# Performance work log

Hardware: AMD Instinct MI355X
Metric: run time of the kernel (lower is better)

Reference implementation:

```python
import jax, jax.numpy as jnp
import numpy as np

N_USERS = 120000
N_ITEMS = 80000
N_NODES = N_USERS + N_ITEMS
D = 64
H = 2
DK = 32
DV = 32
N_LAYERS = 3
N_EDGES = 1280000
B = 4096
TEMPERATURE = 1.0


def setup_inputs() -> dict:
    key = jax.random.key(0)
    ks = jax.random.split(key, 11)
    glorot = lambda k, shape: jax.random.normal(k, shape, dtype=jnp.float32) * np.sqrt(2.0 / (shape[0] + int(np.prod(shape[1:]))))
    return {
        "edge_src": jax.random.randint(ks[0], (N_EDGES,), 0, N_NODES, dtype=jnp.int32),
        "edge_dst": jax.random.randint(ks[1], (N_EDGES,), 0, N_NODES, dtype=jnp.int32),
        # normalized adjacency values (positive, small) like D^-1/2 A D^-1/2 entries
        "edge_val": jax.random.uniform(ks[2], (N_EDGES,), dtype=jnp.float32) * 0.2,
        "U_emb": jax.random.normal(ks[3], (N_USERS, D), dtype=jnp.float32) * 0.01,
        "V_emb": jax.random.normal(ks[4], (N_ITEMS, D), dtype=jnp.float32) * 0.01,
        "Wq": glorot(ks[5], (D, H, DK)),
        "Wk": glorot(ks[6], (D, H, DK)),
        "Wv": glorot(ks[7], (D, H, DV)),
        "Wo": glorot(ks[8], (H * DV, D)),
        "u": jax.random.randint(ks[9], (B,), 0, N_USERS, dtype=jnp.int32),
        "i": jax.random.randint(ks[10], (B,), 0, N_ITEMS, dtype=jnp.int32),
    }


def reference(edge_src, edge_dst, edge_val, U_emb, V_emb, Wq, Wk, Wv, Wo, u, i):
    E0 = jnp.concatenate([U_emb, V_emb], axis=0)  # (N, d)

    # LightGCN propagation: E_{l+1} = A_norm @ E_l via edge-list scatter-add
    def prop(E, _):
        msg = edge_val[:, None] * E[edge_src]                      # (E, d) gather
        En = jax.ops.segment_sum(msg, edge_dst, num_segments=N_NODES)  # (N, d) scatter
        return En, En

    _, layer_outs = jax.lax.scan(prop, E0, None, length=N_LAYERS)
    Es = jnp.concatenate([E0[None], layer_outs], axis=0)  # (L, N, d), L = n_layers+1

    # Layer-wise QKV attention: Q from E0, K/V from every layer
    Q = jnp.einsum('nd,dhk->nhk', E0, Wq)        # (N, H, dk)
    K = jnp.einsum('lnd,dhk->lnhk', Es, Wk)      # (L, N, H, dk)
    V = jnp.einsum('lnd,dhv->lnhv', Es, Wv)      # (L, N, H, dv)
    scale = jnp.sqrt(jnp.asarray(DK, dtype=Q.dtype))
    scores = jnp.einsum('lnhk,nhk->lnh', K, Q) / scale
    alphas = jax.nn.softmax(scores / TEMPERATURE, axis=0)  # softmax over layers
    heads = jnp.einsum('lnh,lnhv->nhv', alphas, V)          # (N, H, dv)
    E_out = heads.reshape(N_NODES, H * DV) @ Wo             # (N, d)

    # score(u, i): dot product of final user/item embeddings
    Ue = E_out[u]
    Ie = E_out[N_USERS + i]
    return jnp.sum(Ue * Ie, axis=1)  # (B,)
```

## Files before the change

### kernel.cpp

```cpp
#include <hip/hip_runtime.h>
#include <hip/hip_fp16.h>

#define NU 120000
#define NI 80000
#define NN 200000
#define DD 64
#define NE 1280000
#define BB 4096
#define NS 8192
#define NB2 196
#define BCAP 8192
#define CH2 4096

#define FB 196
#define CONVB 3125
#define PREPB 64
#define BSB 32
#define P1B 2048
#define G0B 512
#define NLB 32

__global__ void k_pre(int* __restrict__ bcur, int* __restrict__ n2cnt) {
  int t = threadIdx.x;
  if (t < NB2) bcur[t] = 0;
  if (t == 0) *n2cnt = 0;
}

__global__ void k_coarse2(const int* __restrict__ src, const int* __restrict__ dst,
                          const float* __restrict__ val, int* __restrict__ bcur,
                          int2* __restrict__ c_sv) {
  __shared__ int2 sv[CH2];
  __shared__ unsigned char map8[CH2];
  __shared__ int hist[256];
  __shared__ int lbase[256];
  __shared__ int gbase[256];
  __shared__ int s[256];
  int t = threadIdx.x;
  hist[t] = 0;
  __syncthreads();
  int e0 = blockIdx.x * CH2;
  int d_[16];
#pragma unroll
  for (int k = 0; k < 16; ++k) {
    int e = e0 + k * 256 + t;
    d_[k] = (e < NE) ? dst[e] : -1;
    if (d_[k] >= 0) atomicAdd(&hist[d_[k] >> 10], 1);
  }
  __syncthreads();
  int x = hist[t];
  s[t] = x;
  __syncthreads();
  for (int off = 1; off < 256; off <<= 1) {
    int v = (t >= off) ? s[t - off] : 0;
    __syncthreads();
    s[t] += v;
    __syncthreads();
  }
  int lb = s[t] - x;
  lbase[t] = lb;
  gbase[t] = (x && t < NB2) ? (t * BCAP + atomicAdd(&bcur[t], x)) : 0;
  for (int k = lb; k < lb + x; ++k) map8[k] = (unsigned char)t;
  hist[t] = 0;
  __syncthreads();
#pragma unroll
  for (int k = 0; k < 16; ++k) {
    int e = e0 + k * 256 + t;
    if (d_[k] >= 0) {
      int b = d_[k] >> 10;
      int lp = lbase[b] + atomicAdd(&hist[b], 1);
      sv[lp] = make_int2(src[e] | ((d_[k] & 1023) << 18), __float_as_int(val[e]));
    }
  }
  __syncthreads();
  int nval = NE - e0;
  if (nval > CH2) nval = CH2;
  for (int sidx = t; sidx < nval; sidx += 256) {
    int b = map8[sidx];
    c_sv[(size_t)gbase[b] + sidx - lbase[b]] = sv[sidx];
  }
}

__device__ __forceinline__ void d_conv(int rel, const float4* __restrict__ U4,
                                       const float4* __restrict__ V4, uint2* __restrict__ H0) {
  int t = threadIdx.x;
  float4 r[4];
#pragma unroll
  for (int k = 0; k < 4; ++k) {
    int idx = rel * 1024 + k * 256 + t;
    int node = idx >> 4, q = idx & 15;
    r[k] = (node < NU) ? U4[(size_t)node * 16 + q] : V4[(size_t)(node - NU) * 16 + q];
  }
#pragma unroll
  for (int k = 0; k < 4; ++k) {
    int idx = rel * 1024 + k * 256 + t;
    __half2 a = __floats2half2_rn(r[k].x, r[k].y);
    __half2 b = __floats2half2_rn(r[k].z, r[k].w);
    uint2 o;
    o.x = __builtin_bit_cast(unsigned int, a);
    o.y = __builtin_bit_cast(unsigned int, b);
    H0[idx] = o;
  }
}

__device__ __forceinline__ void d_prep(int rel, const float* __restrict__ Wq,
                                       const float* __restrict__ Wk, const float* __restrict__ Wv,
                                       const float* __restrict__ Wo, float* __restrict__ Mt,
                                       float* __restrict__ P) {
  int t = rel * 256 + threadIdx.x;
  if (t < 8192) {
    int h = t >> 12;
    int b = (t >> 6) & 63;
    int j = t & 63;
    float s = 0.f;
    for (int k = 0; k < 32; ++k) s += Wk[j * 64 + h * 32 + k] * Wq[b * 64 + h * 32 + k];
    Mt[h * 4096 + b * 64 + j] = s;
  } else if (t < 16384) {
    int t2 = t - 8192;
    int h = t2 >> 12;
    int d = (t2 >> 6) & 63;
    int j = t2 & 63;
    float s = 0.f;
    for (int v = 0; v < 32; ++v) s += Wv[d * 64 + h * 32 + v] * Wo[(h * 32 + v) * 64 + j];
    P[h * 4096 + d * 64 + j] = s;
  }
}

__global__ void k_fine4m(const int* __restrict__ bcur, const int2* __restrict__ c_sv,
                         int2* __restrict__ pairs, int* __restrict__ row_ptr,
                         const float4* __restrict__ U4, const float4* __restrict__ V4,
                         uint2* __restrict__ H0, const float* __restrict__ Wq,
                         const float* __restrict__ Wk, const float* __restrict__ Wv,
                         const float* __restrict__ Wo, float* __restrict__ Mt,
                         float* __restrict__ P, const int* __restrict__ u,
                         const int* __restrict__ ii, int* __restrict__ snodes) {
  __shared__ int cnt[1024];
  __shared__ int pre[1024];
  __shared__ int cur[1024];
  __shared__ int s[256];
  __shared__ int bs[256];
  int b = blockIdx.x, t = threadIdx.x;
  if (b >= FB) {
    int r = b - FB;
    if (r < CONVB) {
      d_conv(r, U4, V4, H0);
    } else if (r < CONVB + PREPB) {
      d_prep(r - CONVB, Wq, Wk, Wv, Wo, Mt, P);
    } else {
      int tt = (r - CONVB - PREPB) * 256 + t;
      if (tt < NS) snodes[tt] = (tt < BB) ? u[tt] : NU + ii[tt - BB];
    }
    return;
  }
  int bc = (t < NB2) ? bcur[t] : 0;
  bs[t] = bc;
  __syncthreads();
  for (int off = 1; off < 256; off <<= 1) {
    int v = (t >= off) ? bs[t - off] : 0;
    __syncthreads();
    bs[t] += v;
    __syncthreads();
  }
  int segN = bcur[b];
  int out0 = bs[b] - segN;
  int seg0 = b * BCAP;
  for (int k = t; k < 1024; k += 256) cnt[k] = 0;
  __syncthreads();
  for (int e = t; e < segN; e += 256) atomicAdd(&cnt[(c_sv[seg0 + e].x >> 18) & 1023], 1);
  __syncthreads();
  int a0 = cnt[4 * t], a1 = cnt[4 * t + 1], a2 = cnt[4 * t + 2], a3 = cnt[4 * t + 3];
  int tot = a0 + a1 + a2 + a3;
  s[t] = tot;
  __syncthreads();
  for (int off = 1; off < 256; off <<= 1) {
    int v = (t >= off) ? s[t - off] : 0;
    __syncthreads();
    s[t] += v;
    __syncthreads();
  }
  int base = s[t] - tot;
  pre[4 * t] = base;
  pre[4 * t + 1] = base + a0;
  pre[4 * t + 2] = base + a0 + a1;
  pre[4 * t + 3] = base + a0 + a1 + a2;
  int node0 = b << 10;
#pragma unroll
  for (int k = 0; k < 4; ++k) {
    int n = node0 + 4 * t + k;
    if (n < NN) row_ptr[n] = out0 + pre[4 * t + k];
  }
  if (b == 0 && t == 0) row_ptr[NN] = NE;
  for (int k = t; k < 1024; k += 256) cur[k] = 0;
  __syncthreads();
  for (int e = t; e < segN; e += 256) {
    int2 svv = c_sv[seg0 + e];
    int ld = (svv.x >> 18) & 1023;
    int off = atomicAdd(&cur[ld], 1);
    pairs[out0 + pre[ld] + off] = make_int2(svv.x & 0x3FFFF, svv.y);
  }
}

template <int ULIST, int BYPOS, int OUTF32>
__device__ __forceinline__ void d_prop(const uint2* __restrict__ Hin, uint2* __restrict__ Hout,
                                       float4* __restrict__ Fout,
                                       const int* __restrict__ row_ptr,
                                       const int2* __restrict__ pairs,
                                       const int* __restrict__ list,
                                       const int* __restrict__ countp, int cconst, int relbid,
                                       int nblk) {
  int n = countp ? *countp : cconst;
  int lane = threadIdx.x & 63;
  int c = lane & 15;
  int sl = c & 7;
  int gstride = (nblk * 256) >> 4;
  for (int gid = (relbid * 256 + (int)threadIdx.x) >> 4; gid < n; gid += gstride) {
    int node = ULIST ? list[gid] : gid;
    int start = row_ptr[node], end = row_ptr[node + 1];
    float4 acc = make_float4(0.f, 0.f, 0.f, 0.f);
    for (int t0 = start; t0 < end; t0 += 8) {
      int cap = end - t0;
      if (cap > 8) cap = 8;
      int2 mp = pairs[t0 + (sl < cap ? sl : 0)];
      uint2 r[8];
      float vv[8];
#pragma unroll
      for (int k = 0; k < 8; ++k) {
        int srclane = (lane & 48) + k;
        int sidx = __shfl(mp.x, srclane);
        float v = __int_as_float(__shfl(mp.y, srclane));
        vv[k] = (k < cap) ? v : 0.f;
        r[k] = Hin[(size_t)sidx * 16 + c];
      }
#pragma unroll
      for (int k = 0; k < 8; ++k) {
        float2 f0 = __half22float2(__builtin_bit_cast(__half2, r[k].x));
        float2 f1 = __half22float2(__builtin_bit_cast(__half2, r[k].y));
        acc.x += vv[k] * f0.x;
        acc.y += vv[k] * f0.y;
        acc.z += vv[k] * f1.x;
        acc.w += vv[k] * f1.y;
      }
    }
    size_t op = BYPOS ? (size_t)gid : (size_t)node;
    if (OUTF32) {
      Fout[op * 16 + c] = acc;
    } else {
      __half2 a = __floats2half2_rn(acc.x, acc.y);
      __half2 bq = __floats2half2_rn(acc.z, acc.w);
      uint2 o;
      o.x = __builtin_bit_cast(unsigned int, a);
      o.y = __builtin_bit_cast(unsigned int, bq);
      Hout[op * 16 + c] = o;
    }
  }
}

__device__ __forceinline__ void d_gather_h(int rel, const uint2* __restrict__ Htab,
                                           float4* __restrict__ Es_l,
                                           const int* __restrict__ snodes) {
  int t = rel * 256 + threadIdx.x;
  if (t >= NS * 16) return;
  int p = t >> 4, q = t & 15;
  int node = snodes[p];
  uint2 r = Htab[(size_t)node * 16 + q];
  float2 f0 = __half22float2(__builtin_bit_cast(__half2, r.x));
  float2 f1 = __half22float2(__builtin_bit_cast(__half2, r.y));
  Es_l[p * 16 + q] = make_float4(f0.x, f0.y, f1.x, f1.y);
}

__global__ void k_prop1m(const uint2* __restrict__ H0, uint2* __restrict__ H1,
                         const float4* __restrict__ U4, const float4* __restrict__ V4,
                         float4* __restrict__ Es0, const int* __restrict__ snodes,
                         const int* __restrict__ row_ptr, const int2* __restrict__ pairs,
                         int* __restrict__ n2list, int* __restrict__ n2cnt) {
  int b = blockIdx.x;
  if (b < P1B) {
    d_prop<0, 0, 0>(H0, H1, nullptr, row_ptr, pairs, nullptr, nullptr, NN, b, P1B);
  } else if (b < P1B + G0B) {
    int t = (b - P1B) * 256 + threadIdx.x;
    if (t < NS * 16) {
      int p = t >> 4, q = t & 15;
      int node = snodes[p];
      Es0[p * 16 + q] =
          (node < NU) ? U4[(size_t)node * 16 + q] : V4[(size_t)(node - NU) * 16 + q];
    }
  } else {
    int idx = (b - P1B - G0B) * 256 + threadIdx.x;
    if (idx < NS) {
      int node = snodes[idx];
      int s0 = row_ptr[node], e0 = row_ptr[node + 1];
      int pos = atomicAdd(n2cnt, e0 - s0 + 1);
      n2list[pos++] = node;
      for (int j = s0; j < e0; ++j) n2list[pos++] = pairs[j].x;
    }
  }
}

__global__ void k_stage2(const uint2* __restrict__ H1, uint2* __restrict__ H2,
                         float4* __restrict__ Es1, const int* __restrict__ snodes,
                         const int* __restrict__ row_ptr, const int2* __restrict__ pairs,
                         const int* __restrict__ n2list, const int* __restrict__ n2cnt) {
  int b = blockIdx.x;
  if (b < 512) {
    d_gather_h(b, H1, Es1, snodes);
  } else {
    d_prop<1, 0, 0>(H1, H2, nullptr, row_ptr, pairs, n2list, n2cnt, 0, b - 512, 1024);
  }
}

__global__ void k_stage3(const uint2* __restrict__ H2, float4* __restrict__ Es2,
                         float4* __restrict__ Es3, const int* __restrict__ snodes,
                         const int* __restrict__ row_ptr, const int2* __restrict__ pairs) {
  int b = blockIdx.x;
  if (b < 512) {
    d_gather_h(b, H2, Es2, snodes);
  } else {
    d_prop<1, 1, 1>(H2, nullptr, Es3, row_ptr, pairs, snodes, nullptr, NS, b - 512, 512);
  }
}

__global__ void k_attn3(const float* __restrict__ Es, const float* __restrict__ Mt,
                        const float* __restrict__ P, float* __restrict__ out) {
  __shared__ float sb[4][3 * 64];
  int wv = threadIdx.x >> 6, lane = threadIdx.x & 63;
  int w = blockIdx.x * 4 + wv;
  if (w >= BB) return;
  const float inv_scale = 0.17677669529663687f;
  const float* M0 = Mt;
  const float* M1 = Mt + 4096;
  const float* P0 = P;
  const float* P1 = P + 4096;
  float eo[2];
#pragma unroll
  for (int side = 0; side < 2; ++side) {
    int p = side ? (BB + w) : w;
    float e0 = Es[(size_t)0 * NS * DD + p * DD + lane];
    float e1 = Es[(size_t)1 * NS * DD + p * DD + lane];
    float e2 = Es[(size_t)2 * NS * DD + p * DD + lane];
    float e3 = Es[(size_t)3 * NS * DD + p * DD + lane];
    sb[wv][lane] = e0;

    float g0 = 0.f, g1 = 0.f;
#pragma unroll 8
    for (int b = 0; b < 64; ++b) {
      float eb = sb[wv][b];
      g0 = fmaf(M0[b * 64 + lane], eb, g0);
      g1 = fmaf(M1[b * 64 + lane], eb, g1);
    }

    float el[4] = {e0, e1, e2, e3};
    float sc[4][2];
#pragma unroll
    for (int l = 0; l < 4; ++l) {
      float p0 = el[l] * g0, p1 = el[l] * g1;
#pragma unroll
      for (int o = 32; o; o >>= 1) {
        p0 += __shfl_xor(p0, o);
        p1 += __shfl_xor(p1, o);
      }
      sc[l][0] = p0 * inv_scale;
      sc[l][1] = p1 * inv_scale;
    }

    float ebar[2];
#pragma unroll
    for (int h = 0; h < 2; ++h) {
      float m = fmaxf(fmaxf(sc[0][h], sc[1][h]), fmaxf(sc[2][h], sc[3][h]));
      float x0 = expf(sc[0][h] - m), x1 = expf(sc[1][h] - m);
      float x2 = expf(sc[2][h] - m), x3 = expf(sc[3][h] - m);
      float inv = 1.f / (x0 + x1 + x2 + x3);
      ebar[h] = (x0 * e0 + x1 * e1 + x2 * e2 + x3 * e3) * inv;
    }
    sb[wv][64 + lane] = ebar[0];
    sb[wv][128 + lane] = ebar[1];

    float o = 0.f;
#pragma unroll 8
    for (int d = 0; d < 64; ++d) {
      float b0 = sb[wv][64 + d];
      float b1 = sb[wv][128 + d];
      o = fmaf(P0[d * 64 + lane], b0, o);
      o = fmaf(P1[d * 64 + lane], b1, o);
    }
    eo[side] = o;
  }
  float pd = eo[0] * eo[1];
#pragma unroll
  for (int o = 32; o; o >>= 1) pd += __shfl_xor(pd, o);
  if (lane == 0) out[w] = pd;
}

extern "C" void kernel_launch(void* const* d_in, const int* in_sizes, int n_in,
                              void* d_out, int out_size, void* d_ws, size_t ws_size,
                              hipStream_t stream) {
  const int* edge_src = (const int*)d_in[0];
  const int* edge_dst = (const int*)d_in[1];
  const float* edge_val = (const float*)d_in[2];
  const float* U_emb = (const float*)d_in[3];
  const float* V_emb = (const float*)d_in[4];
  const float* Wq = (const float*)d_in[5];
  const float* Wk = (const float*)d_in[6];
  const float* Wv = (const float*)d_in[7];
  const float* Wo = (const float*)d_in[8];
  const int* u = (const int*)d_in[9];
  const int* ii = (const int*)d_in[10];
  float* out = (float*)d_out;

  const float4* U4 = (const float4*)U_emb;
  const float4* V4 = (const float4*)V_emb;

  float* Ea = (float*)d_ws;
  float* Eb = Ea + (size_t)NN * DD;
  float* Es = Eb + (size_t)NN * DD;
  float* Mt = Es + (size_t)4 * NS * DD;
  float* Pm = Mt + 8192;
  int* row_ptr = (int*)(Pm + 8192);
  int* bcur = row_ptr + NN + 4;
  int* snodes = bcur + NB2;
  int* n2cnt = snodes + NS;
  uintptr_t pa = (uintptr_t)(n2cnt + 1);
  pa = (pa + 15) & ~(uintptr_t)15;
  int2* pairs = (int2*)pa;

  uint2* H0 = (uint2*)Ea;
  uint2* H1 = H0 + (size_t)NN * 16;
  uint2* H2 = (uint2*)Eb;
  int2* c_sv = (int2*)Eb;
  int* n2list = (int*)(Es + (size_t)3 * NS * DD);

  float4* Es4 = (float4*)Es;

  k_pre<<<1, 256, 0, stream>>>(bcur, n2cnt);
  k_coarse2<<<(NE + CH2 - 1) / CH2, 256, 0, stream>>>(edge_src, edge_dst, edge_val, bcur, c_sv);
  k_fine4m<<<FB + CONVB + PREPB + BSB, 256, 0, stream>>>(bcur, c_sv, pairs, row_ptr, U4, V4, H0,
                                                         Wq, Wk, Wv, Wo, Mt, Pm, u, ii, snodes);
  k_prop1m<<<P1B + G0B + NLB, 256, 0, stream>>>(H0, H1, U4, V4, Es4 + (size_t)0 * NS * 16, snodes,
                                                row_ptr, pairs, n2list, n2cnt);
  k_stage2<<<512 + 1024, 256, 0, stream>>>(H1, H2, Es4 + (size_t)1 * NS * 16, snodes, row_ptr,
                                           pairs, n2list, n2cnt);
  k_stage3<<<512 + 512, 256, 0, stream>>>(H2, Es4 + (size_t)2 * NS * 16,
                                          Es4 + (size_t)3 * NS * 16, snodes, row_ptr, pairs);
  k_attn3<<<(BB + 3) / 4, 256, 0, stream>>>(Es, Mt, Pm, out);
}
```

Baseline: 132.8 us.

## Widen propagation gathers to 16-byte loads with 8 lanes per node

The SpMM propagation now assigns 8 lanes per node instead of 16, and each lane loads a uint4 (8 halves) per neighbour row rather than a uint2. This doubles the number of nodes processed per wavefront and halves the number of gather instructions, at the cost of more registers per lane. Separately, the coarse binning chunk is halved to 2048 edges, which launches twice as many k_coarse2 blocks.

After: 134.7 us. About the same (+1.5%).

```diff
diff --git a/kernel.cpp b/kernel.cpp
--- a/kernel.cpp
+++ b/kernel.cpp
@@ -10,7 +10,8 @@
 #define NS 8192
 #define NB2 196
 #define BCAP 8192
-#define CH2 4096
+#define CH2 2048
+#define CB 625
 
 #define FB 196
 #define CONVB 3125
@@ -39,9 +40,9 @@
   hist[t] = 0;
   __syncthreads();
   int e0 = blockIdx.x * CH2;
-  int d_[16];
-#pragma unroll
-  for (int k = 0; k < 16; ++k) {
+  int d_[CH2 / 256];
+#pragma unroll
+  for (int k = 0; k < CH2 / 256; ++k) {
     int e = e0 + k * 256 + t;
     d_[k] = (e < NE) ? dst[e] : -1;
     if (d_[k] >= 0) atomicAdd(&hist[d_[k] >> 10], 1);
@@ -63,7 +64,7 @@
   hist[t] = 0;
   __syncthreads();
 #pragma unroll
-  for (int k = 0; k < 16; ++k) {
+  for (int k = 0; k < CH2 / 256; ++k) {
     int e = e0 + k * 256 + t;
     if (d_[k] >= 0) {
       int b = d_[k] >> 10;
@@ -200,56 +201,64 @@
 }
 
 template <int ULIST, int BYPOS, int OUTF32>
-__device__ __forceinline__ void d_prop(const uint2* __restrict__ Hin, uint2* __restrict__ Hout,
-                                       float4* __restrict__ Fout,
-                                       const int* __restrict__ row_ptr,
-                                       const int2* __restrict__ pairs,
-                                       const int* __restrict__ list,
-                                       const int* __restrict__ countp, int cconst, int relbid,
-                                       int nblk) {
+__device__ __forceinline__ void d_prop8(const uint4* __restrict__ Hin4,
+                                        uint4* __restrict__ Hout4, float4* __restrict__ Fout,
+                                        const int* __restrict__ row_ptr,
+                                        const int2* __restrict__ pairs,
+                                        const int* __restrict__ list,
+                                        const int* __restrict__ countp, int cconst, int relbid,
+                                        int nblk) {
   int n = countp ? *countp : cconst;
   int lane = threadIdx.x & 63;
-  int c = lane & 15;
-  int sl = c & 7;
-  int gstride = (nblk * 256) >> 4;
-  for (int gid = (relbid * 256 + (int)threadIdx.x) >> 4; gid < n; gid += gstride) {
+  int c = lane & 7;
+  int gb = lane & 56;
+  int gstride = (nblk * 256) >> 3;
+  for (int gid = (relbid * 256 + (int)threadIdx.x) >> 3; gid < n; gid += gstride) {
     int node = ULIST ? list[gid] : gid;
     int start = row_ptr[node], end = row_ptr[node + 1];
-    float4 acc = make_float4(0.f, 0.f, 0.f, 0.f);
+    float4 a0 = make_float4(0.f, 0.f, 0.f, 0.f);
+    float4 a1 = make_float4(0.f, 0.f, 0.f, 0.f);
     for (int t0 = start; t0 < end; t0 += 8) {
       int cap = end - t0;
       if (cap > 8) cap = 8;
-      int2 mp = pairs[t0 + (sl < cap ? sl : 0)];
-      uint2 r[8];
+      int2 mp = pairs[t0 + (c < cap ? c : 0)];
+      uint4 r[8];
       float vv[8];
 #pragma unroll
       for (int k = 0; k < 8; ++k) {
-        int srclane = (lane & 48) + k;
+        int srclane = gb + k;
         int sidx = __shfl(mp.x, srclane);
         float v = __int_as_float(__shfl(mp.y, srclane));
         vv[k] = (k < cap) ? v : 0.f;
-        r[k] = Hin[(size_t)sidx * 16 + c];
+        r[k] = Hin4[(size_t)sidx * 8 + c];
       }
 #pragma unroll
       for (int k = 0; k < 8; ++k) {
         float2 f0 = __half22float2(__builtin_bit_cast(__half2, r[k].x));
         float2 f1 = __half22float2(__builtin_bit_cast(__half2, r[k].y));
-        acc.x += vv[k] * f0.x;
-        acc.y += vv[k] * f0.y;
-        acc.z += vv[k] * f1.x;
-        acc.w += vv[k] * f1.y;
+        float2 f2 = __half22float2(__builtin_bit_cast(__half2, r[k].z));
+        float2 f3 = __half22float2(__builtin_bit_cast(__half2, r[k].w));
+        a0.x += vv[k] * f0.x;
+        a0.y += vv[k] * f0.y;
+        a0.z += vv[k] * f1.x;
+        a0.w += vv[k] * f1.y;
+        a1.x += vv[k] * f2.x;
+        a1.y += vv[k] * f2.y;
+        a1.z += vv[k] * f3.x;
+        a1.w += vv[k] * f3.y;
       }
     }
     size_t op = BYPOS ? (size_t)gid : (size_t)node;
     if (OUTF32) {
-      Fout[op * 16 + c] = acc;
+      Fout[op * 16 + 2 * c] = a0;
+      Fout[op * 16 + 2 * c + 1] = a1;
     } else {
-      __half2 a = __floats2half2_rn(acc.x, acc.y);
-      __half2 bq = __floats2half2_rn(acc.z, acc.w);
-      uint2 o;
-      o.x = __builtin_bit_cast(unsigned int, a);
-      o.y = __builtin_bit_cast(unsigned int, bq);
-      Hout[op * 16 + c] = o;
+      uint4 o;
+      o.x = __builtin_bit_cast(unsigned int, __floats2half2_rn(a0.x, a0.y));
+      o.y = __builtin_bit_cast(unsigned int, __floats2half2_rn(a0.z, a0.w));
+      o.z = __builtin_bit_cast(unsigned int, __floats2half2_rn(a1.x, a1.y));
+      o.w = __builtin_bit_cast(unsigned int, __floats2half2_rn(a1.z, a1.w));
+      Hout4[op * 8 + c] = o;
     }
   }
 }
@@ -267,14 +276,14 @@
   Es_l[p * 16 + q] = make_float4(f0.x, f0.y, f1.x, f1.y);
 }
 
-__global__ void k_prop1m(const uint2* __restrict__ H0, uint2* __restrict__ H1,
+__global__ void k_prop1m(const uint4* __restrict__ H04, uint4* __restrict__ H14,
                          const float4* __restrict__ U4, const float4* __restrict__ V4,
                          float4* __restrict__ Es0, const int* __restrict__ snodes,
                          const int* __restrict__ row_ptr, const int2* __restrict__ pairs,
                          int* __restrict__ n2list, int* __restrict__ n2cnt) {
   int b = blockIdx.x;
   if (b < P1B) {
-    d_prop<0, 0, 0>(H0, H1, nullptr, row_ptr, pairs, nullptr, nullptr, NN, b, P1B);
+    d_prop8<0, 0, 0>(H04, H14, nullptr, row_ptr, pairs, nullptr, nullptr, NN, b, P1B);
   } else if (b < P1B + G0B) {
     int t = (b - P1B) * 256 + threadIdx.x;
     if (t < NS * 16) {
@@ -295,26 +304,28 @@
   }
 }
 
-__global__ void k_stage2(const uint2* __restrict__ H1, uint2* __restrict__ H2,
-                         float4* __restrict__ Es1, const int* __restrict__ snodes,
-                         const int* __restrict__ row_ptr, const int2* __restrict__ pairs,
-                         const int* __restrict__ n2list, const int* __restrict__ n2cnt) {
+__global__ void k_stage2(const uint4* __restrict__ H14, uint4* __restrict__ H24,
+                         const uint2* __restrict__ H1, float4* __restrict__ Es1,
+                         const int* __restrict__ snodes, const int* __restrict__ row_ptr,
+                         const int2* __restrict__ pairs, const int* __restrict__ n2list,
+                         const int* __restrict__ n2cnt) {
   int b = blockIdx.x;
   if (b < 512) {
     d_gather_h(b, H1, Es1, snodes);
   } else {
-    d_prop<1, 0, 0>(H1, H2, nullptr, row_ptr, pairs, n2list, n2cnt, 0, b - 512, 1024);
-  }
-}
-
-__global__ void k_stage3(const uint2* __restrict__ H2, float4* __restrict__ Es2,
-                         float4* __restrict__ Es3, const int* __restrict__ snodes,
-                         const int* __restrict__ row_ptr, const int2* __restrict__ pairs) {
+    d_prop8<1, 0, 0>(H14, H24, nullptr, row_ptr, pairs, n2list, n2cnt, 0, b - 512, 1024);
+  }
+}
+
+__global__ void k_stage3(const uint4* __restrict__ H24, const uint2* __restrict__ H2,
+                         float4* __restrict__ Es2, float4* __restrict__ Es3,
+                         const int* __restrict__ snodes, const int* __restrict__ row_ptr,
+                         const int2* __restrict__ pairs) {
   int b = blockIdx.x;
   if (b < 512) {
     d_gather_h(b, H2, Es2, snodes);
   } else {
-    d_prop<1, 1, 1>(H2, nullptr, Es3, row_ptr, pairs, snodes, nullptr, NS, b - 512, 512);
+    d_prop8<1, 1, 1>(H24, nullptr, Es3, row_ptr, pairs, snodes, nullptr, NS, b - 512, 512);
   }
 }
 
@@ -430,14 +441,16 @@
   float4* Es4 = (float4*)Es;
 
   k_pre<<<1, 256, 0, stream>>>(bcur, n2cnt);
-  k_coarse2<<<(NE + CH2 - 1) / CH2, 256, 0, stream>>>(edge_src, edge_dst, edge_val, bcur, c_sv);
+  k_coarse2<<<CB, 256, 0, stream>>>(edge_src, edge_dst, edge_val, bcur, c_sv);
   k_fine4m<<<FB + CONVB + PREPB + BSB, 256, 0, stream>>>(bcur, c_sv, pairs, row_ptr, U4, V4, H0,
                                                          Wq, Wk, Wv, Wo, Mt, Pm, u, ii, snodes);
-  k_prop1m<<<P1B + G0B + NLB, 256, 0, stream>>>(H0, H1, U4, V4, Es4 + (size_t)0 * NS * 16, snodes,
-                                                row_ptr, pairs, n2list, n2cnt);
-  k_stage2<<<512 + 1024, 256, 0, stream>>>(H1, H2, Es4 + (size_t)1 * NS * 16, snodes, row_ptr,
-                                           pairs, n2list, n2cnt);
-  k_stage3<<<512 + 512, 256, 0, stream>>>(H2, Es4 + (size_t)2 * NS * 16,
+  k_prop1m<<<P1B + G0B + NLB, 256, 0, stream>>>((const uint4*)H0, (uint4*)H1, U4, V4,
+                                                Es4 + (size_t)0 * NS * 16, snodes, row_ptr, pairs,
+                                                n2list, n2cnt);
+  k_stage2<<<512 + 1024, 256, 0, stream>>>((const uint4*)H1, (uint4*)H2, H1,
+                                           Es4 + (size_t)1 * NS * 16, snodes, row_ptr, pairs,
+                                           n2list, n2cnt);
+  k_stage3<<<512 + 512, 256, 0, stream>>>((const uint4*)H2, H2, Es4 + (size_t)2 * NS * 16,
                                           Es4 + (size_t)3 * NS * 16, snodes, row_ptr, pairs);
   k_attn3<<<(BB + 3) / 4, 256, 0, stream>>>(Es, Mt, Pm, out);
 }
```
